# Kernel tuning notes

Hardware: AMD Instinct MI355X
Metric: run time of the kernel (lower is better)

## Reference

```python
import jax, jax.numpy as jnp
import numpy as np

B, H, W, CIN, COUT = 16, 256, 256, 64, 64
M1, M2 = 32, 32  # retained Fourier modes; M2 <= W//2+1


def setup_inputs() -> dict:
    key = jax.random.key(0)
    k0, k1, k2, k3, k4 = jax.random.split(key, 5)
    # complex_scale = sqrt(2/(Cin+Cout)) / sqrt(2), per module default init
    cscale = (2.0 / (CIN + COUT)) ** 0.5 / 2.0 ** 0.5
    x = jax.random.normal(k0, (B, H, W, CIN), jnp.float32)
    wshape = (CIN, COUT, M1, M2)
    w1_re = cscale * jax.random.normal(k1, wshape, jnp.float32)
    w1_im = cscale * jax.random.normal(k2, wshape, jnp.float32)
    w2_re = cscale * jax.random.normal(k3, wshape, jnp.float32)
    w2_im = cscale * jax.random.normal(k4, wshape, jnp.float32)
    bias = jnp.zeros((COUT,), jnp.float32)
    return {"x": x, "w1_re": w1_re, "w1_im": w1_im,
            "w2_re": w2_re, "w2_im": w2_im, "bias": bias}


def reference(x, w1_re, w1_im, w2_re, w2_im, bias):
    # x: (B,H,W,Cin) -> rfft over spatial axes, norm='forward'
    x_ft = jnp.fft.rfftn(x, axes=(1, 2), norm='forward')  # (B,H,W//2+1,Cin) c64
    w1 = jax.lax.complex(w1_re, w1_im)  # (Cin,Cout,M1,M2)
    w2 = jax.lax.complex(w2_re, w2_im)
    # two corners: low-positive and low-negative frequencies along axis 1
    top = jnp.einsum('bxyi,ioxy->bxyo', x_ft[:, :M1, :M2, :], w1)
    bot = jnp.einsum('bxyi,ioxy->bxyo', x_ft[:, -M1:, :M2, :], w2)
    out_ft = jnp.zeros((B, H, W // 2 + 1, COUT), dtype=jnp.complex64)
    out_ft = out_ft.at[:, :M1, :M2, :].set(top)
    out_ft = out_ft.at[:, -M1:, :M2, :].set(bot)
    out = jnp.fft.irfftn(out_ft, s=(H, W), axes=(1, 2), norm='forward')
    return out + bias.reshape(1, 1, 1, COUT)
```

## Files before the change

kernel.cpp:

```cpp
#include <hip/hip_runtime.h>
#include <math.h>

#define NB 16
#define NH 256
#define NW 256
#define TWO_PI 6.28318530717958647692f
#define FSCALE (1.0f/65536.0f)

#define OFF_X  ((size_t)1 << 23)
#define OFF_OF (((size_t)1 << 23) + ((size_t)1 << 21))
#define WS_FLOATS_NEEDED (((size_t)1 << 23) + ((size_t)2 << 21))

typedef __attribute__((ext_vector_type(8))) short short8;
typedef __attribute__((ext_vector_type(4))) float f32x4;

__device__ __forceinline__ unsigned short f2bf(float f) {
    unsigned int u = __float_as_uint(f);
    unsigned int r = (u + 0x7FFFu + ((u >> 16) & 1u)) >> 16;
    return (unsigned short)r;
}
__device__ __forceinline__ float bf2f(unsigned int u16) {
    return __uint_as_float(u16 << 16);
}
__device__ __forceinline__ unsigned int pk2(float a, float b) {
    return (unsigned int)f2bf(a) | ((unsigned int)f2bf(b) << 16);
}

#define XPITCH 264
__global__ __launch_bounds__(256) void k1_dft_w(const float* __restrict__ x,
                                                float* __restrict__ WS) {
    __shared__ float2 tw[256];
    __shared__ unsigned short Al[64 * XPITCH];
    __shared__ unsigned short Xl[64 * XPITCH];
    int t = threadIdx.x;
    { float s, c; sincosf(TWO_PI * (float)t * (1.0f/256.0f), &s, &c);
      tw[t] = make_float2(c, s); }
    __syncthreads();
    {
        int m  = t >> 2;
        int w0 = (t & 3) * 64;
        int ky = m & 31;
        for (int dw8 = 0; dw8 < 8; ++dw8) {
            short8 v8;
#pragma unroll
            for (int j = 0; j < 8; ++j) {
                int w = w0 + dw8*8 + j;
                float2 cs = tw[(ky * w) & 255];
                float v = (m < 32) ? cs.x : -cs.y;
                v8[j] = (short)f2bf(v * FSCALE);
            }
            *(short8*)&Al[m * XPITCH + w0 + dw8*8] = v8;
        }
    }
    int wave = t >> 6, lane = t & 63;
    int col = lane & 15, kq = lane >> 4;
    unsigned int* Gu = (unsigned int*)WS;
    for (int u = 0; u < 4; ++u) {
        int bh = blockIdx.x * 4 + u;
        __syncthreads();
        {
            const float* xs = x + (size_t)bh * 16384 + t * 64;
            for (int i4 = 0; i4 < 16; ++i4) {
                float4 v = *(const float4*)(xs + i4*4);
                Xl[(i4*4+0)*XPITCH + t] = f2bf(v.x);
                Xl[(i4*4+1)*XPITCH + t] = f2bf(v.y);
                Xl[(i4*4+2)*XPITCH + t] = f2bf(v.z);
                Xl[(i4*4+3)*XPITCH + t] = f2bf(v.w);
            }
        }
        __syncthreads();
        f32x4 acc[4];
#pragma unroll
        for (int n = 0; n < 4; ++n) acc[n] = (f32x4){0.f, 0.f, 0.f, 0.f};
#pragma unroll
        for (int kk = 0; kk < 8; ++kk) {
            int k = kk*32 + kq*8;
            short8 af = *(const short8*)&Xl[(wave*16 + col) * XPITCH + k];
#pragma unroll
            for (int n = 0; n < 4; ++n) {
                short8 bf = *(const short8*)&Al[(n*16 + col) * XPITCH + k];
                acc[n] = __builtin_amdgcn_mfma_f32_16x16x32_bf16(af, bf, acc[n], 0, 0, 0);
            }
        }
        int i0 = wave*16 + kq*4;
        unsigned int* gp = Gu + (size_t)bh * 2048;
#pragma unroll
        for (int g = 0; g < 2; ++g) {
            int ky = g*16 + col;
            uint4 pk;
            pk.x = pk2(acc[g][0], acc[g+2][0]);
            pk.y = pk2(acc[g][1], acc[g+2][1]);
            pk.z = pk2(acc[g][2], acc[g+2][2]);
            pk.w = pk2(acc[g][3], acc[g+2][3]);
            *(uint4*)(gp + ky*64 + i0) = pk;
        }
    }
}

#define K2P 264
__global__ __launch_bounds__(1024) void k2_dft_h(float* __restrict__ WS) {
    int b  = blockIdx.x >> 5;
    int ky = blockIdx.x & 31;
    int t  = threadIdx.x;
    __shared__ float2 tw[256];
    __shared__ unsigned short A2l[64 * K2P];
    __shared__ unsigned short B1l[64 * K2P];
    __shared__ unsigned short B2l[64 * K2P];
    if (t < 256) { float s, c; sincosf(TWO_PI * (float)t * (1.0f/256.0f), &s, &c);
                   tw[t] = make_float2(c, s); }
    __syncthreads();
    {
        int r = t >> 4, s0 = (t & 15) * 16;
        int kxe = (r < 32) ? r : r + 192;
#pragma unroll
        for (int c8 = 0; c8 < 2; ++c8) {
            short8 v8;
#pragma unroll
            for (int j = 0; j < 8; ++j) {
                int s = s0 + c8*8 + j;
                float v = (s <= 128) ? tw[(kxe * s) & 255].x
                                     : tw[(kxe * (s - 128)) & 255].y;
                v8[j] = (short)f2bf(v);
            }
            *(short8*)&A2l[r*K2P + s0 + c8*8] = v8;
        }
    }
    int i = t & 63, hg = t >> 6;
    const unsigned int* gu = (const unsigned int*)WS
                             + (size_t)(b*256)*2048 + ky*64 + i;
    for (int s2 = 0; hg + 16*s2 <= 128; ++s2) {
        int hp = hg + 16*s2;
        unsigned int ga = gu[(size_t)hp*2048];
        float are = bf2f(ga & 0xffffu), aim = bf2f(ga >> 16);
        if (hp == 0 || hp == 128) {
            B1l[i*K2P + hp] = f2bf(are);
            B2l[i*K2P + hp] = f2bf(aim);
        } else {
            unsigned int gb = gu[(size_t)(256-hp)*2048];
            float bre = bf2f(gb & 0xffffu), bim = bf2f(gb >> 16);
            B1l[i*K2P + hp]       = f2bf(are + bre);
            B1l[i*K2P + 128 + hp] = f2bf(aim - bim);
            B2l[i*K2P + hp]       = f2bf(aim + bim);
            B2l[i*K2P + 128 + hp] = f2bf(bre - are);
        }
    }
    __syncthreads();
    int wave = t >> 6, col = t & 15, kq = (t >> 4) & 3;
    int mt = wave >> 2, n = wave & 3;
    f32x4 ar = (f32x4){0.f,0.f,0.f,0.f}, ai = (f32x4){0.f,0.f,0.f,0.f};
#pragma unroll
    for (int kk = 0; kk < 8; ++kk) {
        int k = kk*32 + kq*8;
        short8 af = *(const short8*)&A2l[(mt*16 + col)*K2P + k];
        short8 b1 = *(const short8*)&B1l[(n*16 + col)*K2P + k];
        short8 b2 = *(const short8*)&B2l[(n*16 + col)*K2P + k];
        ar = __builtin_amdgcn_mfma_f32_16x16x32_bf16(af, b1, ar, 0, 0, 0);
        ai = __builtin_amdgcn_mfma_f32_16x16x32_bf16(af, b2, ai, 0, 0, 0);
    }
    unsigned int* Xu = (unsigned int*)(WS + OFF_X);
#pragma unroll
    for (int q = 0; q < 4; ++q) {
        int kxrow = mt*16 + kq*4 + q;
        Xu[(((size_t)b*64 + kxrow)*32 + ky)*64 + n*16 + col] = pk2(ar[q], ai[q]);
    }
}

__global__ __launch_bounds__(512) void k3_mix(const float* __restrict__ w1re,
                                              const float* __restrict__ w1im,
                                              const float* __restrict__ w2re,
                                              const float* __restrict__ w2im,
                                              float* __restrict__ WS) {
    int kx  = blockIdx.x & 63;
    int kyq = blockIdx.x >> 6;
    int t   = threadIdx.x;
    __shared__ float2 lx[8192];
    __shared__ float  lw[2][2][4][576];
    const float* wre = (kx < 32) ? w1re : w2re;
    const float* wim = (kx < 32) ? w1im : w2im;
    int m = kx & 31;
    const unsigned int* Xu = (const unsigned int*)(WS + OFF_X);
    for (int n = t; n < 8192; n += 512) {
        int bb = n >> 9, ky8 = (n >> 6) & 7, ii = n & 63;
        unsigned int g = Xu[(((size_t)bb*64 + kx)*32 + kyq*8 + ky8)*64 + ii];
        lx[n] = make_float2(bf2f(g & 0xffffu), bf2f(g >> 16));
    }
    int sarr = t & 1, so = (t >> 1) & 63, si4 = t >> 7;
    const float* wsrc = sarr ? wim : wre;
    size_t sbase = (size_t)m*32 + kyq*8;
    int kyl = t >> 6;
    int o   = t & 63;
    int kyg = kyq*8 + kyl;
    float ar[16], ai[16];
#pragma unroll
    for (int bb = 0; bb < 16; ++bb) { ar[bb] = 0.f; ai[bb] = 0.f; }

    float4 wa, wb;
    {
        const float* src = wsrc + ((size_t)(si4*64 + so)*1024 + sbase);
        wa = *(const float4*)src; wb = *(const float4*)(src + 4);
        float* dst = &lw[0][sarr][si4][so*9];
        dst[0]=wa.x; dst[1]=wa.y; dst[2]=wa.z; dst[3]=wa.w;
        dst[4]=wb.x; dst[5]=wb.y; dst[6]=wb.z; dst[7]=wb.w;
    }
    __syncthreads();

    for (int k = 0; k < 16; ++k) {
        int i0 = k*4;
        float4 na, nb;
        if (k < 15) {
            const float* src = wsrc + ((size_t)((i0+4+si4)*64 + so)*1024 + sbase);
            na = *(const float4*)src; nb = *(const float4*)(src + 4);
        }
#pragma unroll
        for (int di = 0; di < 4; ++di) {
            float wr = lw[k & 1][0][di][o*9 + kyl];
            float wi = lw[k & 1][1][di][o*9 + kyl];
            int ii = i0 + di;
#pragma unroll
            for (int bb = 0; bb < 16; ++bb) {
                float2 xv = lx[(bb*8 + kyl)*64 + ii];
                ar[bb] = fmaf(xv.x, wr, fmaf(-xv.y, wi, ar[bb]));
                ai[bb] = fmaf(xv.x, wi, fmaf( xv.y, wr, ai[bb]));
            }
        }
        if (k < 15) {
            float* dst = &lw[(k+1) & 1][sarr][si4][so*9];
            dst[0]=na.x; dst[1]=na.y; dst[2]=na.z; dst[3]=na.w;
            dst[4]=nb.x; dst[5]=nb.y; dst[6]=nb.z; dst[7]=nb.w;
        }
        __syncthreads();
    }
    unsigned int* ofu = (unsigned int*)(WS + OFF_OF);
#pragma unroll
    for (int bb = 0; bb < 16; ++bb) {
        ofu[(((size_t)bb*64 + kx)*32 + kyg)*64 + o] = pk2(ar[bb], ai[bb]);
    }
}

#define K4P 136
__global__ __launch_bounds__(1024) void k4_idft_h(float* __restrict__ WS) {
    int b  = blockIdx.x >> 5;
    int ky = blockIdx.x & 31;
    int t  = threadIdx.x;
    __shared__ float2 tw[256];
    __shared__ unsigned short A4l[256 * K4P];
    __shared__ unsigned short B1l[64 * K4P];
    __shared__ unsigned short B2l[64 * K4P];
    if (t < 256) { float s, c; sincosf(TWO_PI * (float)t * (1.0f/256.0f), &s, &c);
                   tw[t] = make_float2(c, s); }
    __syncthreads();
    {
        int h = t >> 2, s0 = (t & 3) * 32;
#pragma unroll
        for (int c8 = 0; c8 < 4; ++c8) {
            short8 v8;
#pragma unroll
            for (int j = 0; j < 8; ++j) {
                int s = s0 + c8*8 + j;
                int ds = s & 63;
                int kxe = (ds < 32) ? ds : ds + 192;
                float2 cs = tw[(kxe * h) & 255];
                v8[j] = (short)f2bf((s < 64) ? cs.x : cs.y);
            }
            *(short8*)&A4l[h*K4P + s0 + c8*8] = v8;
        }
    }
    int o = t & 63, kg = t >> 6;
    const unsigned int* ofu = (const unsigned int*)(WS + OFF_OF);
#pragma unroll
    for (int s = 0; s < 4; ++s) {
        int kx = kg*4 + s;
        unsigned int g = ofu[(((size_t)b*64 + kx)*32 + ky)*64 + o];
        unsigned short lo = (unsigned short)(g & 0xffffu);
        unsigned short hi = (unsigned short)(g >> 16);
        B1l[o*K4P + kx]      = lo;
        B1l[o*K4P + 64 + kx] = hi ^ 0x8000u;
        B2l[o*K4P + kx]      = hi;
        B2l[o*K4P + 64 + kx] = lo;
    }
    __syncthreads();
    int wave = t >> 6, col = t & 15, kq = (t >> 4) & 3;
    unsigned int* tmpu = (unsigned int*)WS;
#pragma unroll
    for (int e = 0; e < 4; ++e) {
        int p = wave*4 + e, mt = p >> 2, n = p & 3;
        f32x4 ar = (f32x4){0.f,0.f,0.f,0.f}, ai = (f32x4){0.f,0.f,0.f,0.f};
#pragma unroll
        for (int kk = 0; kk < 4; ++kk) {
            int k = kk*32 + kq*8;
            short8 af = *(const short8*)&A4l[(mt*16 + col)*K4P + k];
            short8 b1 = *(const short8*)&B1l[(n*16 + col)*K4P + k];
            short8 b2 = *(const short8*)&B2l[(n*16 + col)*K4P + k];
            ar = __builtin_amdgcn_mfma_f32_16x16x32_bf16(af, b1, ar, 0, 0, 0);
            ai = __builtin_amdgcn_mfma_f32_16x16x32_bf16(af, b2, ai, 0, 0, 0);
        }
#pragma unroll
        for (int q = 0; q < 4; ++q) {
            int h  = mt*16 + kq*4 + q;
            int o2 = n*16 + col;
            tmpu[(size_t)(b*256 + h)*2048 + ky*64 + o2] = pk2(ar[q], ai[q]);
        }
    }
}

#define APITCH 72
__global__ __launch_bounds__(256) void k5_idft_w(const float* __restrict__ bias,
                                                 const float* __restrict__ WS,
                                                 float* __restrict__ out) {
    int t = threadIdx.x;
    __shared__ float2 tw[256];
    __shared__ unsigned short T5[256 * APITCH];
    __shared__ unsigned short Bl[64 * APITCH];
    { float s, c; sincosf(TWO_PI * (float)t * (1.0f/256.0f), &s, &c);
      tw[t] = make_float2(c, s); }
    __syncthreads();
    {
        int w = t;
#pragma unroll
        for (int ky = 0; ky < 32; ++ky) {
            float2 cs = tw[(ky * w) & 255];
            float sc = ky ? 2.f : 1.f;
            T5[w*APITCH + ky]      = f2bf(sc * cs.x);
            T5[w*APITCH + 32 + ky] = f2bf(-sc * cs.y);
        }
    }
    int o = t & 63, kg = t >> 6;
    int wave = t >> 6, col = t & 15, kq = (t >> 4) & 3;
    float bv[4];
#pragma unroll
    for (int n = 0; n < 4; ++n) bv[n] = bias[n*16 + col];

    for (int u = 0; u < 4; ++u) {
        int bh = blockIdx.x * 4 + u;
        __syncthreads();
        {
            const unsigned int* tpu = (const unsigned int*)WS + (size_t)bh * 2048;
#pragma unroll
            for (int kk = 0; kk < 8; ++kk) {
                int ky = kg*8 + kk;
                unsigned int g = tpu[ky*64 + o];
                Bl[o*APITCH + ky]      = (unsigned short)(g & 0xffffu);
                Bl[o*APITCH + 32 + ky] = (unsigned short)(g >> 16);
            }
        }
        __syncthreads();
        f32x4 acc[4][4];
#pragma unroll
        for (int mt = 0; mt < 4; ++mt)
#pragma unroll
            for (int n = 0; n < 4; ++n) acc[mt][n] = (f32x4){0.f,0.f,0.f,0.f};
#pragma unroll
        for (int kk = 0; kk < 2; ++kk) {
            short8 af[4];
#pragma unroll
            for (int mt = 0; mt < 4; ++mt)
                af[mt] = *(const short8*)&T5[(wave*64 + mt*16 + col)*APITCH
                                             + kk*32 + kq*8];
#pragma unroll
            for (int n = 0; n < 4; ++n) {
                short8 bf = *(const short8*)&Bl[(n*16 + col)*APITCH
                                                + kk*32 + kq*8];
#pragma unroll
                for (int mt = 0; mt < 4; ++mt)
                    acc[mt][n] = __builtin_amdgcn_mfma_f32_16x16x32_bf16(
                                     af[mt], bf, acc[mt][n], 0, 0, 0);
            }
        }
        float* R = out + (size_t)bh * 16384;
#pragma unroll
        for (int mt = 0; mt < 4; ++mt)
#pragma unroll
            for (int n = 0; n < 4; ++n)
#pragma unroll
                for (int q = 0; q < 4; ++q) {
                    int w = wave*64 + mt*16 + kq*4 + q;
                    R[w*64 + n*16 + col] = acc[mt][n][q] + bv[n];
                }
    }
}

extern "C" void kernel_launch(void* const* d_in, const int* in_sizes, int n_in,
                              void* d_out, int out_size, void* d_ws, size_t ws_size,
                              hipStream_t stream) {
    (void)in_sizes; (void)n_in; (void)out_size;
    if (ws_size < WS_FLOATS_NEEDED * sizeof(float)) return;
    const float* x    = (const float*)d_in[0];
    const float* w1re = (const float*)d_in[1];
    const float* w1im = (const float*)d_in[2];
    const float* w2re = (const float*)d_in[3];
    const float* w2im = (const float*)d_in[4];
    const float* bias = (const float*)d_in[5];
    float* O  = (float*)d_out;
    float* WS = (float*)d_ws;

    k1_dft_w <<<1024,  256, 0, stream>>>(x, WS);
    k2_dft_h <<< 512, 1024, 0, stream>>>(WS);
    k3_mix   <<< 256,  512, 0, stream>>>(w1re, w1im, w2re, w2im, WS);
    k4_idft_h<<< 512, 1024, 0, stream>>>(WS);
    k5_idft_w<<<1024,  256, 0, stream>>>(bias, WS, O);
}
```

Baseline: 215.5 us.

## Double block size of width-DFT kernels and coalesce input load in k1

Raises k1 and k5 from 256 to 512 threads per block and splits each block's MFMA work across eight waves, so each wave holds fewer accumulators. k1 also changes how x is staged into LDS: each thread reads four rows with float4 loads and writes packed bf16 pairs, replacing the old per-thread strided scalar stores. The aim is more latency hiding on the two memory-bound end stages and cheaper LDS transposes. In exchange, each block carries more threads that must meet at barriers, and some wave-level reuse of A fragments is lost.

```diff
diff --git a/kernel.cpp b/kernel.cpp
--- a/kernel.cpp
+++ b/kernel.cpp
@@ -27,73 +27,77 @@
 }
 
 #define XPITCH 264
-__global__ __launch_bounds__(256) void k1_dft_w(const float* __restrict__ x,
+__global__ __launch_bounds__(512) void k1_dft_w(const float* __restrict__ x,
                                                 float* __restrict__ WS) {
     __shared__ float2 tw[256];
     __shared__ unsigned short Al[64 * XPITCH];
     __shared__ unsigned short Xl[64 * XPITCH];
     int t = threadIdx.x;
-    { float s, c; sincosf(TWO_PI * (float)t * (1.0f/256.0f), &s, &c);
-      tw[t] = make_float2(c, s); }
+    if (t < 256) { float s, c; sincosf(TWO_PI * (float)t * (1.0f/256.0f), &s, &c);
+                   tw[t] = make_float2(c, s); }
     __syncthreads();
     {
-        int m  = t >> 2;
-        int w0 = (t & 3) * 64;
+        int m = t >> 3, w0T = (t & 7) * 32;
         int ky = m & 31;
-        for (int dw8 = 0; dw8 < 8; ++dw8) {
+#pragma unroll
+        for (int d8 = 0; d8 < 4; ++d8) {
             short8 v8;
 #pragma unroll
             for (int j = 0; j < 8; ++j) {
-                int w = w0 + dw8*8 + j;
+                int w = w0T + d8*8 + j;
                 float2 cs = tw[(ky * w) & 255];
                 float v = (m < 32) ? cs.x : -cs.y;
                 v8[j] = (short)f2bf(v * FSCALE);
             }
-            *(short8*)&Al[m * XPITCH + w0 + dw8*8] = v8;
+            *(short8*)&Al[m * XPITCH + w0T + d8*8] = v8;
         }
     }
     int wave = t >> 6, lane = t & 63;
     int col = lane & 15, kq = lane >> 4;
+    int mtile = wave & 3, g = wave >> 2;
+    int wq = t & 15, sub = (t >> 4) & 3;
     unsigned int* Gu = (unsigned int*)WS;
     for (int u = 0; u < 4; ++u) {
         int bh = blockIdx.x * 4 + u;
         __syncthreads();
-        {
-            const float* xs = x + (size_t)bh * 16384 + t * 64;
-            for (int i4 = 0; i4 < 16; ++i4) {
-                float4 v = *(const float4*)(xs + i4*4);
-                Xl[(i4*4+0)*XPITCH + t] = f2bf(v.x);
-                Xl[(i4*4+1)*XPITCH + t] = f2bf(v.y);
-                Xl[(i4*4+2)*XPITCH + t] = f2bf(v.z);
-                Xl[(i4*4+3)*XPITCH + t] = f2bf(v.w);
-            }
+        const float* xb = x + (size_t)bh * 16384;
+#pragma unroll
+        for (int p = 0; p < 2; ++p) {
+            int i0 = (wave + 8*p) * 4;
+            int w0 = sub*64 + wq*4;
+            float4 r0 = *(const float4*)(xb + (w0+0)*64 + i0);
+            float4 r1 = *(const float4*)(xb + (w0+1)*64 + i0);
+            float4 r2 = *(const float4*)(xb + (w0+2)*64 + i0);
+            float4 r3 = *(const float4*)(xb + (w0+3)*64 + i0);
+            uint2 s0; s0.x = pk2(r0.x, r1.x); s0.y = pk2(r2.x, r3.x);
+            *(uint2*)&Xl[(i0+0)*XPITCH + w0] = s0;
+            uint2 s1; s1.x = pk2(r0.y, r1.y); s1.y = pk2(r2.y, r3.y);
+            *(uint2*)&Xl[(i0+1)*XPITCH + w0] = s1;
+            uint2 s2; s2.x = pk2(r0.z, r1.z); s2.y = pk2(r2.z, r3.z);
+            *(uint2*)&Xl[(i0+2)*XPITCH + w0] = s2;
+            uint2 s3; s3.x = pk2(r0.w, r1.w); s3.y = pk2(r2.w, r3.w);
+            *(uint2*)&Xl[(i0+3)*XPITCH + w0] = s3;
         }
         __syncthreads();
-        f32x4 acc[4];
-#pragma unroll
-        for (int n = 0; n < 4; ++n) acc[n] = (f32x4){0.f, 0.f, 0.f, 0.f};
+        f32x4 a0 = (f32x4){0.f,0.f,0.f,0.f};
+        f32x4 a1 = (f32x4){0.f,0.f,0.f,0.f};
 #pragma unroll
         for (int kk = 0; kk < 8; ++kk) {
             int k = kk*32 + kq*8;
-            short8 af = *(const short8*)&Xl[(wave*16 + col) * XPITCH + k];
-#pragma unroll
-            for (int n = 0; n < 4; ++n) {
-                short8 bf = *(const short8*)&Al[(n*16 + col) * XPITCH + k];
-                acc[n] = __builtin_amdgcn_mfma_f32_16x16x32_bf16(af, bf, acc[n], 0, 0, 0);
-            }
-        }
-        int i0 = wave*16 + kq*4;
-        unsigned int* gp = Gu + (size_t)bh * 2048;
-#pragma unroll
-        for (int g = 0; g < 2; ++g) {
-            int ky = g*16 + col;
-            uint4 pk;
-            pk.x = pk2(acc[g][0], acc[g+2][0]);
-            pk.y = pk2(acc[g][1], acc[g+2][1]);
-            pk.z = pk2(acc[g][2], acc[g+2][2]);
-            pk.w = pk2(acc[g][3], acc[g+2][3]);
-            *(uint4*)(gp + ky*64 + i0) = pk;
-        }
+            short8 af = *(const short8*)&Xl[(mtile*16 + col) * XPITCH + k];
+            short8 b0 = *(const short8*)&Al[(g*16 + col) * XPITCH + k];
+            short8 b1 = *(const short8*)&Al[((g+2)*16 + col) * XPITCH + k];
+            a0 = __builtin_amdgcn_mfma_f32_16x16x32_bf16(af, b0, a0, 0, 0, 0);
+            a1 = __builtin_amdgcn_mfma_f32_16x16x32_bf16(af, b1, a1, 0, 0, 0);
+        }
+        int i0s = mtile*16 + kq*4;
+        int ky = g*16 + col;
+        uint4 pk;
+        pk.x = pk2(a0[0], a1[0]);
+        pk.y = pk2(a0[1], a1[1]);
+        pk.z = pk2(a0[2], a1[2]);
+        pk.w = pk2(a0[3], a1[3]);
+        *(uint4*)(Gu + (size_t)bh * 2048 + ky*64 + i0s) = pk;
     }
 }
 
@@ -304,20 +308,21 @@
 }
 
 #define APITCH 72
-__global__ __launch_bounds__(256) void k5_idft_w(const float* __restrict__ bias,
+__global__ __launch_bounds__(512) void k5_idft_w(const float* __restrict__ bias,
                                                  const float* __restrict__ WS,
                                                  float* __restrict__ out) {
     int t = threadIdx.x;
     __shared__ float2 tw[256];
     __shared__ unsigned short T5[256 * APITCH];
     __shared__ unsigned short Bl[64 * APITCH];
-    { float s, c; sincosf(TWO_PI * (float)t * (1.0f/256.0f), &s, &c);
-      tw[t] = make_float2(c, s); }
+    if (t < 256) { float s, c; sincosf(TWO_PI * (float)t * (1.0f/256.0f), &s, &c);
+                   tw[t] = make_float2(c, s); }
     __syncthreads();
     {
-        int w = t;
-#pragma unroll
-        for (int ky = 0; ky < 32; ++ky) {
+        int w = t >> 1, hf = (t & 1) * 16;
+#pragma unroll
+        for (int j = 0; j < 16; ++j) {
+            int ky = hf + j;
             float2 cs = tw[(ky * w) & 255];
             float sc = ky ? 2.f : 1.f;
             T5[w*APITCH + ky]      = f2bf(sc * cs.x);
@@ -336,44 +341,44 @@
         {
             const unsigned int* tpu = (const unsigned int*)WS + (size_t)bh * 2048;
 #pragma unroll
-            for (int kk = 0; kk < 8; ++kk) {
-                int ky = kg*8 + kk;
+            for (int kk = 0; kk < 4; ++kk) {
+                int ky = kg*4 + kk;
                 unsigned int g = tpu[ky*64 + o];
                 Bl[o*APITCH + ky]      = (unsigned short)(g & 0xffffu);
                 Bl[o*APITCH + 32 + ky] = (unsigned short)(g >> 16);
             }
         }
         __syncthreads();
-        f32x4 acc[4][4];
-#pragma unroll
-        for (int mt = 0; mt < 4; ++mt)
+        f32x4 acc[2][4];
+#pragma unroll
+        for (int mt = 0; mt < 2; ++mt)
 #pragma unroll
             for (int n = 0; n < 4; ++n) acc[mt][n] = (f32x4){0.f,0.f,0.f,0.f};
 #pragma unroll
         for (int kk = 0; kk < 2; ++kk) {
-            short8 af[4];
-#pragma unroll
-            for (int mt = 0; mt < 4; ++mt)
-                af[mt] = *(const short8*)&T5[(wave*64 + mt*16 + col)*APITCH
+            short8 af[2];
+#pragma unroll
+            for (int mt = 0; mt < 2; ++mt)
+                af[mt] = *(const short8*)&T5[(wave*32 + mt*16 + col)*APITCH
                                              + kk*32 + kq*8];
 #pragma unroll
             for (int n = 0; n < 4; ++n) {
                 short8 bf = *(const short8*)&Bl[(n*16 + col)*APITCH
                                                 + kk*32 + kq*8];
 #pragma unroll
-                for (int mt = 0; mt < 4; ++mt)
+                for (int mt = 0; mt < 2; ++mt)
                     acc[mt][n] = __builtin_amdgcn_mfma_f32_16x16x32_bf16(
                                      af[mt], bf, acc[mt][n], 0, 0, 0);
             }
         }
         float* R = out + (size_t)bh * 16384;
 #pragma unroll
-        for (int mt = 0; mt < 4; ++mt)
+        for (int mt = 0; mt < 2; ++mt)
 #pragma unroll
             for (int n = 0; n < 4; ++n)
 #pragma unroll
                 for (int q = 0; q < 4; ++q) {
-                    int w = wave*64 + mt*16 + kq*4 + q;
+                    int w = wave*32 + mt*16 + kq*4 + q;
                     R[w*64 + n*16 + col] = acc[mt][n][q] + bv[n];
                 }
     }
@@ -393,9 +398,9 @@
     float* O  = (float*)d_out;
     float* WS = (float*)d_ws;
 
-    k1_dft_w <<<1024,  256, 0, stream>>>(x, WS);
+    k1_dft_w <<<1024,  512, 0, stream>>>(x, WS);
     k2_dft_h <<< 512, 1024, 0, stream>>>(WS);
     k3_mix   <<< 256,  512, 0, stream>>>(w1re, w1im, w2re, w2im, WS);
     k4_idft_h<<< 512, 1024, 0, stream>>>(WS);
-    k5_idft_w<<<1024,  256, 0, stream>>>(bias, WS, O);
-}
+    k5_idft_w<<<1024,  512, 0, stream>>>(bias, WS, O);
+}
```

Result: slower. 235.0 us (+9.0%).
